# Optimization experiments

Hardware: AMD Instinct MI355X
Metric: run time of the kernel (lower is better)

## Reference

```python
import jax, jax.numpy as jnp
import numpy as np

T_STEP, NUM_PATCHES = 16, 49
DIM, MLP_DIM, HEADS, DEPTH = 512, 2048, 8, 4
PATCH_DIM = 432
N_BATCH = 32
NEG = -1e9
EPS = 1e-5


def _ln(x, g, b):
    m = x.mean(-1, keepdims=True)
    v = ((x - m) ** 2).mean(-1, keepdims=True)
    return (x - m) / jnp.sqrt(v + EPS) * g + b


def setup_inputs() -> dict:
    key = jax.random.key(0)
    ks = jax.random.split(key, 16)
    L = T_STEP * NUM_PATCHES
    s = 0.02
    return {
        "patch": jax.random.normal(ks[0], (N_BATCH, L, PATCH_DIM), jnp.float32),
        "done": jax.random.randint(ks[1], (N_BATCH, T_STEP - 1), 0, 2).astype(jnp.int32),
        "W_embed": jax.random.normal(ks[2], (PATCH_DIM, DIM), jnp.float32) * s,
        "b_embed": jnp.zeros((DIM,), jnp.float32),
        "spatial_embed": jax.random.normal(ks[3], (1, NUM_PATCHES, DIM), jnp.float32),
        "temporal_embed": jax.random.normal(ks[4], (1, T_STEP, DIM), jnp.float32),
        "ln1_g": jnp.ones((DEPTH, DIM), jnp.float32),
        "ln1_b": jnp.zeros((DEPTH, DIM), jnp.float32),
        "Wqkv": jax.random.normal(ks[5], (DEPTH, DIM, 3 * DIM), jnp.float32) * s,
        "bqkv": jnp.zeros((DEPTH, 3 * DIM), jnp.float32),
        "Wo": jax.random.normal(ks[6], (DEPTH, DIM, DIM), jnp.float32) * s,
        "bo": jnp.zeros((DEPTH, DIM), jnp.float32),
        "ln2_g": jnp.ones((DEPTH, DIM), jnp.float32),
        "ln2_b": jnp.zeros((DEPTH, DIM), jnp.float32),
        "W1": jax.random.normal(ks[7], (DEPTH, DIM, MLP_DIM), jnp.float32) * s,
        "b1": jnp.zeros((DEPTH, MLP_DIM), jnp.float32),
        "W2": jax.random.normal(ks[8], (DEPTH, MLP_DIM, DIM), jnp.float32) * s,
        "b2": jnp.zeros((DEPTH, DIM), jnp.float32),
        "out_g": jnp.ones((DIM,), jnp.float32),
        "out_b": jnp.zeros((DIM,), jnp.float32),
    }


def reference(patch, done, W_embed, b_embed, spatial_embed, temporal_embed,
              ln1_g, ln1_b, Wqkv, bqkv, Wo, bo, ln2_g, ln2_b,
              W1, b1, W2, b2, out_g, out_b):
    N, L, _ = patch.shape
    # patch embed + factored pos embed
    x = patch @ W_embed + b_embed
    pos = jnp.tile(spatial_embed, (1, T_STEP, 1)) + jnp.repeat(temporal_embed, NUM_PATCHES, axis=1)
    x = x + pos
    # episodic attention mask: done_mask[n,t] = 1 iff any done[n, c]==1 for c >= t
    d = done.astype(jnp.float32)  # (N, T-1)
    dm = (jnp.flip(jnp.cumsum(jnp.flip(d, 1), 1), 1) > 0).astype(jnp.float32)
    dm = jnp.concatenate([dm, jnp.zeros((N, 1), jnp.float32)], axis=1)  # (N, T)
    pm = jnp.repeat(dm, NUM_PATCHES, axis=1)  # (N, L)
    keep = 1.0 - pm
    mask = 1.0 - keep[:, :, None] * keep[:, None, :]  # (N, L, L); 1 = blocked
    bias = jnp.where(mask > 0.5, NEG, 0.0)[:, None, :, :]  # (N, 1, L, L)
    dh = DIM // HEADS
    scale = dh ** -0.5
    for i in range(DEPTH):
        h = _ln(x, ln1_g[i], ln1_b[i])
        qkv = h @ Wqkv[i] + bqkv[i]
        q, k, v = jnp.split(qkv, 3, axis=-1)
        q = q.reshape(N, L, HEADS, dh).transpose(0, 2, 1, 3)
        k = k.reshape(N, L, HEADS, dh).transpose(0, 2, 1, 3)
        v = v.reshape(N, L, HEADS, dh).transpose(0, 2, 1, 3)
        scores = jnp.einsum('nhqd,nhkd->nhqk', q, k) * scale + bias
        attn = jax.nn.softmax(scores, axis=-1)
        o = jnp.einsum('nhqk,nhkd->nhqd', attn, v)
        o = o.transpose(0, 2, 1, 3).reshape(N, L, DIM)
        x = x + (o @ Wo[i] + bo[i])
        h = _ln(x, ln2_g[i], ln2_b[i])
        x = x + (jax.nn.gelu(h @ W1[i] + b1[i], approximate=False) @ W2[i] + b2[i])
    return _ln(x, out_g, out_b)
```

## Files before the change

### kernel.cpp

```cpp
#include <hip/hip_runtime.h>
#include <math.h>

#define NB 32
#define LQ 784
#define LQP 832
#define DIM 512
#define HEADS 8
#define MLP 2048
#define KPAD 448
#define MROWS 25088

typedef __attribute__((ext_vector_type(8))) short s8v;
typedef __attribute__((ext_vector_type(4))) short s4v;
typedef __attribute__((ext_vector_type(4))) float f4v;

__device__ __forceinline__ short f2b(float f){
  unsigned u = __builtin_bit_cast(unsigned, f);
  u = (u + 0x7fffu + ((u >> 16) & 1u)) >> 16;
  return (short)u;
}
__device__ __forceinline__ float b2f(short s){
  unsigned u = ((unsigned)(unsigned short)s) << 16;
  return __builtin_bit_cast(float, u);
}

__device__ __forceinline__ void gll16(const short* g, short* l){
  __builtin_amdgcn_global_load_lds(
      (const __attribute__((address_space(1))) void*)g,
      (__attribute__((address_space(3))) void*)l, 16, 0, 0);
}

__device__ __forceinline__ void xcd_remap(int &bm, int &bn, int gx, int gy){
  int nwg = gx * gy;
  int flat = bm * gx + bn;
  int xcd = flat & 7, idx = flat >> 3;
  int q = nwg >> 3, r = nwg & 7;
  int nf = (xcd < r ? xcd * (q + 1) : r * (q + 1) + (xcd - r) * q) + idx;
  bm = nf / gx;
  bn = nf - bm * gx;
}

__global__ __launch_bounds__(512) void mask_k(const int* __restrict__ done, float* __restrict__ keepL,
                                              int* __restrict__ kmask, int* __restrict__ liveg){
  __shared__ float keep[32][16];
  int tid = threadIdx.x;
  { int n = tid >> 4, t = tid & 15;
    int any = 0;
    for (int c = t; c < 15; ++c) any |= done[n*15 + c];
    keep[n][t] = any ? 0.f : 1.f; }
  __syncthreads();
  for (int i = tid; i < NB*LQP; i += 512){
    int n = i / LQP, l = i - n*LQP;
    keepL[i] = (l < LQ) ? keep[n][l/49] : 0.f;
  }
  if (tid < 32){
    int n = tid, m = 0;
    for (int kb = 0; kb < 13; ++kb){
      int t0 = (kb*64)/49, t1 = (kb*64 + 63)/49; if (t1 > 15) t1 = 15;
      float a = 0.f;
      for (int t = t0; t <= t1; ++t) a += keep[n][t];
      if (a > 0.5f) m |= 1 << kb;
    }
    kmask[n] = m;
  }
  for (int g = tid; g < 392; g += 512){
    float a = 0.f;
    for (int i2 = 0; i2 < 64; ++i2){
      int row = g*64 + i2;
      int n = row / 784, l = row - n*784;
      a += keep[n][l/49];
    }
    liveg[g] = a > 0.5f ? 1 : 0;
  }
}

__global__ __launch_bounds__(256) void zpad_k(short* __restrict__ Qb, short* __restrict__ Kb,
                                              short* __restrict__ Vtb){
  int idx = blockIdx.x*256 + threadIdx.x;
  s8v z;
  #pragma unroll
  for (int e=0;e<8;++e) z[e] = 0;
  if (idx < 98304){
    int nh = idx / 384, r = idx - nh*384;
    *(s8v*)(Qb + (long)nh*LQP*64 + 784*64 + r*8) = z;
  } else if (idx < 196608){
    int i2 = idx - 98304; int nh = i2 / 384, r = i2 - nh*384;
    *(s8v*)(Kb + (long)nh*LQP*64 + 784*64 + r*8) = z;
  } else {
    int i2 = idx - 196608; int nh = i2 / 384, rem = i2 - nh*384, d = rem/6, s = rem - d*6;
    *(s8v*)(Vtb + ((long)nh*64 + d)*LQP + 784 + s*8) = z;
  }
}

__global__ __launch_bounds__(256) void vmean_k(const short* __restrict__ Vtb, float* __restrict__ Vm){
  int nh = blockIdx.x;
  int tid = threadIdx.x;
  int d = tid >> 2, seg = tid & 3;
  const short* row = Vtb + ((long)nh*64 + d)*LQP;
  float s = 0.f;
  for (int c = seg; c < 98; c += 4){
    s8v v = *(const s8v*)(row + c*8);
    #pragma unroll
    for (int e=0;e<8;++e) s += b2f(v[e]);
  }
  s += __shfl_xor(s, 1, 64);
  s += __shfl_xor(s, 2, 64);
  if (seg == 0) Vm[nh*64 + d] = s * (1.0f/784.0f);
}

__device__ __forceinline__ void transp_body(long idx, const float* __restrict__ src,
                                            short* __restrict__ dst, int R, int C, int Rpad,
                                            long sStride, long dStride){
  long per = (long)C * Rpad;
  int z = (int)(idx / per);
  long rem = idx - (long)z * per;
  int cc = (int)(rem / Rpad);
  int r  = (int)(rem - (long)cc * Rpad);
  short v = 0;
  if (r < R) v = f2b(src[(long)z * sStride + (long)r * C + cc]);
  dst[(long)z * dStride + rem] = v;
}

#define PB0 43904
#define PB1 896
#define PB2 12288
#define PB3 4096
#define PB4 16384
#define PB5 16384

__global__ __launch_bounds__(256) void prep_k(
    const float* __restrict__ patch, short* __restrict__ patchb,
    const float* __restrict__ Wemb, short* __restrict__ Wembt,
    const float* __restrict__ Wqkv, short* __restrict__ Wqkvt,
    const float* __restrict__ Wo, short* __restrict__ Wot,
    const float* __restrict__ W1, short* __restrict__ W1t,
    const float* __restrict__ W2, short* __restrict__ W2t){
  int b = blockIdx.x;
  int tid = threadIdx.x;
  if (b < PB0){
    long idx = (long)b*256 + tid;
    if (idx >= (long)MROWS*KPAD) return;
    int r = (int)(idx / KPAD);
    int c = (int)(idx - (long)r*KPAD);
    patchb[idx] = (c < 432) ? f2b(patch[(long)r*432 + c]) : (short)0;
  } else if (b < PB0+PB1){
    long idx = (long)(b-PB0)*256 + tid;
    if (idx < 229376) transp_body(idx, Wemb, Wembt, 432, 512, 448, 0, 0);
  } else if (b < PB0+PB1+PB2){
    long idx = (long)(b-PB0-PB1)*256 + tid;
    if (idx < 3145728) transp_body(idx, Wqkv, Wqkvt, 512, 1536, 512, 512L*1536, 1536L*512);
  } else if (b < PB0+PB1+PB2+PB3){
    long idx = (long)(b-PB0-PB1-PB2)*256 + tid;
    if (idx < 1048576) transp_body(idx, Wo, Wot, 512, 512, 512, 512L*512, 512L*512);
  } else if (b < PB0+PB1+PB2+PB3+PB4){
    long idx = (long)(b-PB0-PB1-PB2-PB3)*256 + tid;
    if (idx < 4194304) transp_body(idx, W1, W1t, 512, 2048, 512, 512L*2048, 2048L*512);
  } else {
    long idx = (long)(b-PB0-PB1-PB2-PB3-PB4)*256 + tid;
    if (idx < 4194304) transp_body(idx, W2, W2t, 2048, 512, 2048, 2048L*512, 512L*2048);
  }
}

__global__ __launch_bounds__(256) void ln_k(const float* __restrict__ x, const float* __restrict__ g,
                                            const float* __restrict__ b, short* __restrict__ outb,
                                            float* __restrict__ outf){
  int lane = threadIdx.x & 63;
  long row = (long)blockIdx.x * 4 + (threadIdx.x >> 6);
  const float* xr = x + row * DIM + lane * 8;
  float va[8];
  { float4 t0 = *(const float4*)xr; float4 t1 = *(const float4*)(xr + 4);
    va[0]=t0.x; va[1]=t0.y; va[2]=t0.z; va[3]=t0.w;
    va[4]=t1.x; va[5]=t1.y; va[6]=t1.z; va[7]=t1.w; }
  float s = 0.f, q = 0.f;
  #pragma unroll
  for (int j=0;j<8;++j){ s += va[j]; q += va[j]*va[j]; }
  #pragma unroll
  for (int m=1;m<64;m<<=1){ s += __shfl_xor(s,m,64); q += __shfl_xor(q,m,64); }
  float mean = s * (1.0f/DIM);
  float var = q * (1.0f/DIM) - mean*mean;
  float inv = rsqrtf(var + 1e-5f);
  int cb = lane*8;
  if (outb){
    s8v o;
    #pragma unroll
    for (int j=0;j<8;++j) o[j] = f2b((va[j]-mean)*inv*g[cb+j] + b[cb+j]);
    *(s8v*)(outb + row*DIM + cb) = o;
  } else {
    float4 t0, t1;
    t0.x=(va[0]-mean)*inv*g[cb+0]+b[cb+0]; t0.y=(va[1]-mean)*inv*g[cb+1]+b[cb+1];
    t0.z=(va[2]-mean)*inv*g[cb+2]+b[cb+2]; t0.w=(va[3]-mean)*inv*g[cb+3]+b[cb+3];
    t1.x=(va[4]-mean)*inv*g[cb+4]+b[cb+4]; t1.y=(va[5]-mean)*inv*g[cb+5]+b[cb+5];
    t1.z=(va[6]-mean)*inv*g[cb+6]+b[cb+6]; t1.w=(va[7]-mean)*inv*g[cb+7]+b[cb+7];
    *(float4*)(outf + row*DIM + cb) = t0;
    *(float4*)(outf + row*DIM + cb + 4) = t1;
  }
}

template<int EPI>
__global__ __launch_bounds__(256) void gemm_k(
    const short* __restrict__ A, const short* __restrict__ Bt,
    const float* __restrict__ bias, int K, int N,
    float* __restrict__ xres, short* __restrict__ outb,
    const float* __restrict__ sp, const float* __restrict__ tp,
    short* __restrict__ Qb, short* __restrict__ Kb, short* __restrict__ Vtb,
    const int* __restrict__ liveg)
{
  __shared__ __align__(16) short lA[2][128*64];
  __shared__ __align__(16) short lB[2][128*64];
  int bm = blockIdx.y, bn = blockIdx.x;
  xcd_remap(bm, bn, gridDim.x, gridDim.y);
  if (EPI == 1){
    if (bn < 8 && liveg[2*bm] == 0 && liveg[2*bm+1] == 0) return;
  }
  int tid = threadIdx.x;
  int lane = tid & 63, wid = tid >> 6;
  int col = lane & 15, quad = lane >> 4;
  int wm = (wid >> 1) * 64, wn = (wid & 1) * 64;
  f4v acc[4][4];
  #pragma unroll
  for (int i=0;i<4;++i)
    #pragma unroll
    for (int j=0;j<4;++j)
      #pragma unroll
      for (int e=0;e<4;++e) acc[i][j][e] = 0.0f;
  const short* Abase = A + (long)bm*128*K;
  const short* Bbase = Bt + (long)bn*128*K;
  int nt = K >> 6;
  #pragma unroll
  for (int c = 0; c < 4; ++c){
    int v = c*256 + tid;
    int r = v >> 3, j = v & 7;
    int kc = (j ^ (r & 7)) * 8;
    gll16(Abase + (long)r*K + kc, lA[0] + v*8);
    gll16(Bbase + (long)r*K + kc, lB[0] + v*8);
  }
  for (int t = 0; t < nt; ++t){
    int cur = t & 1;
    __builtin_amdgcn_s_barrier();
    __builtin_amdgcn_sched_barrier(0);
    if (t + 1 < nt){
      int kt = (t + 1) << 6;
      #pragma unroll
      for (int c = 0; c < 4; ++c){
        int v = c*256 + tid;
        int r = v >> 3, j = v & 7;
        int kc = (j ^ (r & 7)) * 8;
        gll16(Abase + (long)r*K + kt + kc, lA[cur^1] + v*8);
        gll16(Bbase + (long)r*K + kt + kc, lB[cur^1] + v*8);
      }
      asm volatile("s_waitcnt vmcnt(8)" ::: "memory");
    } else {
      asm volatile("s_waitcnt vmcnt(0)" ::: "memory");
    }
    __builtin_amdgcn_s_barrier();
    __builtin_amdgcn_sched_barrier(0);
    __builtin_amdgcn_s_setprio(1);
    #pragma unroll
    for (int ks = 0; ks < 2; ++ks){
      s8v af[4], bf[4];
      #pragma unroll
      for (int j=0;j<4;++j)
        af[j] = *(const s8v*)&lA[cur][(wm + j*16 + col)*64 + (((ks*4+quad) ^ (col&7)))*8];
      #pragma unroll
      for (int i=0;i<4;++i)
        bf[i] = *(const s8v*)&lB[cur][(wn + i*16 + col)*64 + (((ks*4+quad) ^ (col&7)))*8];
      #pragma unroll
      for (int i=0;i<4;++i)
        #pragma unroll
        for (int j=0;j<4;++j)
          acc[i][j] = __builtin_amdgcn_mfma_f32_16x16x32_bf16(bf[i], af[j], acc[i][j], 0, 0, 0);
    }
    __builtin_amdgcn_s_setprio(0);
    __builtin_amdgcn_sched_barrier(0);
  }
  #pragma unroll
  for (int j=0;j<4;++j){
    int grow = (int)bm*128 + wm + j*16 + col;
    int l = 0, t = 0, p = 0, n = 0;
    if (EPI == 0){ l = grow % LQ; t = l / 49; p = l - t*49; }
    if (EPI == 1){ n = grow / LQ; l = grow - n*LQ; }
    #pragma unroll
    for (int i=0;i<4;++i){
      int gc0 = (int)bn*128 + wn + i*16 + quad*4;
      float4 b4 = *(const float4*)(bias + gc0);
      float v0 = acc[i][j][0] + b4.x;
      float v1 = acc[i][j][1] + b4.y;
      float v2 = acc[i][j][2] + b4.z;
      float v3 = acc[i][j][3] + b4.w;
      if (EPI == 0){
        float4 s4 = *(const float4*)(sp + p*DIM + gc0);
        float4 t4 = *(const float4*)(tp + t*DIM + gc0);
        float4 o; o.x = v0 + s4.x + t4.x; o.y = v1 + s4.y + t4.y;
        o.z = v2 + s4.z + t4.z; o.w = v3 + s4.w + t4.w;
        *(float4*)(xres + (long)grow*DIM + gc0) = o;
      } else if (EPI == 1){
        if (gc0 < 512){
          int hh = gc0 >> 6, d0 = gc0 & 63;
          s4v o; o[0]=f2b(v0); o[1]=f2b(v1); o[2]=f2b(v2); o[3]=f2b(v3);
          *(s4v*)(Qb + (((long)(n*HEADS + hh))*LQP + l)*64 + d0) = o;
        } else if (gc0 < 1024){
          int c2 = gc0 - 512; int hh = c2 >> 6, d0 = c2 & 63;
          s4v o; o[0]=f2b(v0); o[1]=f2b(v1); o[2]=f2b(v2); o[3]=f2b(v3);
          *(s4v*)(Kb + (((long)(n*HEADS + hh))*LQP + l)*64 + d0) = o;
        } else {
          int c2 = gc0 - 1024; int hh = c2 >> 6, d0 = c2 & 63;
          long base = ((long)(n*HEADS + hh))*64;
          Vtb[(base + d0+0)*LQP + l] = f2b(v0);
          Vtb[(base + d0+1)*LQP + l] = f2b(v1);
          Vtb[(base + d0+2)*LQP + l] = f2b(v2);
          Vtb[(base + d0+3)*LQP + l] = f2b(v3);
        }
      } else if (EPI == 2){
        float4 xo = *(const float4*)(xres + (long)grow*DIM + gc0);
        xo.x += v0; xo.y += v1; xo.z += v2; xo.w += v3;
        *(float4*)(xres + (long)grow*DIM + gc0) = xo;
      } else if (EPI == 3){
        float g0 = v0 / (1.0f + __expf(-1.595769122f * v0 * (1.0f + 0.044715f*v0*v0)));
        float g1 = v1 / (1.0f + __expf(-1.595769122f * v1 * (1.0f + 0.044715f*v1*v1)));
        float g2 = v2 / (1.0f + __expf(-1.595769122f * v2 * (1.0f + 0.044715f*v2*v2)));
        float g3 = v3 / (1.0f + __expf(-1.595769122f * v3 * (1.0f + 0.044715f*v3*v3)));
        s4v o; o[0]=f2b(g0); o[1]=f2b(g1); o[2]=f2b(g2); o[3]=f2b(g3);
        *(s4v*)(outb + (long)grow*MLP + gc0) = o;
      }
    }
  }
}

__global__ __launch_bounds__(256) void attn_k(
    const short* __restrict__ Qb, const short* __restrict__ Kb,
    const short* __restrict__ Vtb, const float* __restrict__ keepL,
    const int* __restrict__ kmask, const float* __restrict__ Vm,
    short* __restrict__ Ob)
{
  __shared__ __align__(16) short lK[64*64];
  __shared__ __align__(16) short lV[64*64];
  __shared__ __align__(16) short lP[4][16*72];
  int tid = threadIdx.x;
  int lane = tid & 63, wid = tid >> 6;
  int col = lane & 15, quad = lane >> 4;
  int qb = blockIdx.x, h = blockIdx.y, n = blockIdx.z;
  long nh = (long)n*HEADS + h;
  int smask = kmask[n];
  int qr0 = qb*64 + wid*16;
  float vmv[4];
  #pragma unroll
  for (int j=0;j<4;++j) vmv[j] = Vm[nh*64 + j*16 + col];

  if (!((smask >> qb) & 1)){
    #pragma unroll
    for (int j=0;j<4;++j){
      short ov = f2b(vmv[j]);
      #pragma unroll
      for (int r=0;r<4;++r){
        int l = qr0 + quad*4 + r;
        if (l < LQ) Ob[((long)n*LQ + l)*DIM + h*64 + j*16 + col] = ov;
      }
    }
    return;
  }

  const float* kl = keepL + n*LQP;
  const short* qp = Qb + (nh*LQP + qr0 + col)*64 + quad*8;
  s8v aq0 = *(const s8v*)qp;
  s8v aq1 = *(const s8v*)(qp + 32);
  float keepA = kl[qr0 + col];
  if (keepA < 0.5f){
    #pragma unroll
    for (int e=0;e<8;++e){ aq0[e] = 0; aq1[e] = 0; }
  }
  float keepQ[4];
  #pragma unroll
  for (int r=0;r<4;++r) keepQ[r] = kl[qr0 + quad*4 + r];
  float kqs = keepQ[0] + keepQ[1] + keepQ[2] + keepQ[3];
  bool wlive = __ballot(kqs > 0.5f) != 0ull;
  float lsum[4] = {0.f,0.f,0.f,0.f};
  f4v Oacc[4];
  #pragma unroll
  for (int j=0;j<4;++j)
    #pragma unroll
    for (int e=0;e<4;++e) Oacc[j][e] = 0.0f;

  for (int kb = 0; kb < 13; ++kb){
    if (!((smask >> kb) & 1)) continue;
    int kbase = kb*64;
    __syncthreads();
    #pragma unroll
    for (int c = 0; c < 2; ++c){
      int v = c*256 + tid;
      int r = v >> 3, j = v & 7;
      int kc = (j ^ (r & 7)) * 8;
      gll16(Kb + (nh*LQP + kbase + r)*64 + kc, lK + v*8);
    }
    #pragma unroll
    for (int c = 0; c < 2; ++c){
      int v = c*256 + tid;
      int d = v >> 3, j = v & 7;
      int c8 = (j ^ (d & 7)) * 8;
      gll16(Vtb + (nh*64 + d)*LQP + kbase + c8, lV + v*8);
    }
    __syncthreads();
    if (!wlive) continue;
    float pm[4][4];
    #pragma unroll
    for (int ct = 0; ct < 4; ++ct){
      float keepK = kl[kbase + ct*16 + col];
      f4v s;
      #pragma unroll
      for (int e=0;e<4;++e) s[e] = 0.0f;
      #pragma unroll
      for (int ks = 0; ks < 2; ++ks){
        s8v bk = *(const s8v*)&lK[(ct*16 + col)*64 + (((ks*4+quad) ^ (col&7)))*8];
        if (keepK < 0.5f){
          #pragma unroll
          for (int e=0;e<8;++e) bk[e] = 0;
        }
        s = __builtin_amdgcn_mfma_f32_16x16x32_bf16(ks ? aq1 : aq0, bk, s, 0, 0, 0);
      }
      #pragma unroll
      for (int r=0;r<4;++r){
        float a = keepQ[r] * keepK;
        float t = fmaf(s[r], 0.125f, 10000.0f);
        float p = __expf(fmaf(a, t, -10000.0f));
        pm[ct][r] = p;
        lsum[r] += p;
      }
    }
    #pragma unroll
    for (int ct=0; ct<4; ++ct)
      #pragma unroll
      for (int r=0;r<4;++r)
        lP[wid][(quad*4 + r)*72 + ct*16 + col] = f2b(pm[ct][r]);
    #pragma unroll
    for (int j=0;j<4;++j){
      #pragma unroll
      for (int ks=0; ks<2; ++ks){
        s8v ap = *(const s8v*)&lP[wid][col*72 + ks*32 + quad*8];
        s8v bv = *(const s8v*)&lV[(j*16 + col)*64 + (((ks*4+quad) ^ (col&7)))*8];
        Oacc[j] = __builtin_amdgcn_mfma_f32_16x16x32_bf16(ap, bv, Oacc[j], 0, 0, 0);
      }
    }
  }
  #pragma unroll
  for (int m=1; m<16; m<<=1){
    #pragma unroll
    for (int r=0;r<4;++r) lsum[r] += __shfl_xor(lsum[r], m, 64);
  }
  float invl[4];
  #pragma unroll
  for (int r=0;r<4;++r) invl[r] = 1.0f / lsum[r];
  #pragma unroll
  for (int j=0;j<4;++j)
    #pragma unroll
    for (int r=0;r<4;++r){
      int l = qr0 + quad*4 + r;
      if (l < LQ){
        float val = keepQ[r] > 0.5f ? Oacc[j][r] * invl[r] : vmv[j];
        Ob[((long)n*LQ + l)*DIM + h*64 + j*16 + col] = f2b(val);
      }
    }
}

extern "C" void kernel_launch(void* const* d_in, const int* in_sizes, int n_in,
                              void* d_out, int out_size, void* d_ws, size_t ws_size,
                              hipStream_t stream) {
  const float* patch    = (const float*)d_in[0];
  const int*   done     = (const int*)d_in[1];
  const float* W_embed  = (const float*)d_in[2];
  const float* b_embed  = (const float*)d_in[3];
  const float* spatial  = (const float*)d_in[4];
  const float* temporal = (const float*)d_in[5];
  const float* ln1_g    = (const float*)d_in[6];
  const float* ln1_b    = (const float*)d_in[7];
  const float* Wqkv     = (const float*)d_in[8];
  const float* bqkv     = (const float*)d_in[9];
  const float* Wo       = (const float*)d_in[10];
  const float* bo       = (const float*)d_in[11];
  const float* ln2_g    = (const float*)d_in[12];
  const float* ln2_b    = (const float*)d_in[13];
  const float* W1       = (const float*)d_in[14];
  const float* b1       = (const float*)d_in[15];
  const float* W2       = (const float*)d_in[16];
  const float* b2       = (const float*)d_in[17];
  const float* out_g    = (const float*)d_in[18];
  const float* out_b    = (const float*)d_in[19];
  float* out = (float*)d_out;

  char* ws = (char*)d_ws;
  size_t off = 0;
  auto alloc = [&](size_t bytes)->char*{ char* p = ws + off; off += (bytes + 255) & ~(size_t)255; return p; };
  const size_t QKV_B = (size_t)NB*HEADS*LQP*64*2;
  float* x    = (float*)alloc((size_t)MROWS*DIM*4);
  short* hbuf = (short*)alloc((size_t)MROWS*DIM*2);
  char*  U    = alloc((size_t)MROWS*MLP*2);
  short* patchb = (short*)U;
  short* Qb   = (short*)U;
  short* Kbf  = (short*)(U + QKV_B);
  short* Vtb  = (short*)(U + 2*QKV_B);
  short* obuf = hbuf;
  short* mid  = (short*)U;
  short* Wembt = (short*)alloc((size_t)512*448*2);
  short* Wqkvt = (short*)alloc((size_t)4*1536*512*2);
  short* Wot   = (short*)alloc((size_t)4*512*512*2);
  short* W1t   = (short*)alloc((size_t)4*2048*512*2);
  short* W2t   = (short*)alloc((size_t)4*512*2048*2);
  float* keepL = (float*)alloc((size_t)NB*LQP*4);
  int*   kmask = (int*)alloc(NB*4);
  int*   liveg = (int*)alloc(392*4);
  float* Vm    = (float*)alloc((size_t)NB*HEADS*64*4);

  mask_k<<<1, 512, 0, stream>>>(done, keepL, kmask, liveg);
  prep_k<<<PB0+PB1+PB2+PB3+PB4+PB5, 256, 0, stream>>>(
      patch, patchb, W_embed, Wembt, Wqkv, Wqkvt, Wo, Wot, W1, W1t, W2, W2t);

  gemm_k<0><<<dim3(DIM/128, MROWS/128), 256, 0, stream>>>(
      patchb, Wembt, b_embed, KPAD, DIM, x, nullptr, spatial, temporal,
      nullptr, nullptr, nullptr, nullptr);

  zpad_k<<<1152, 256, 0, stream>>>(Qb, Kbf, Vtb);

  for (int i = 0; i < 4; ++i){
    ln_k<<<MROWS/4, 256, 0, stream>>>(x, ln1_g + i*DIM, ln1_b + i*DIM, hbuf, nullptr);
    gemm_k<1><<<dim3(1536/128, MROWS/128), 256, 0, stream>>>(
        hbuf, Wqkvt + (size_t)i*1536*512, bqkv + (size_t)i*1536, DIM, 1536,
        nullptr, nullptr, nullptr, nullptr, Qb, Kbf, Vtb, liveg);
    vmean_k<<<NB*HEADS, 256, 0, stream>>>(Vtb, Vm);
    attn_k<<<dim3(13, HEADS, NB), 256, 0, stream>>>(Qb, Kbf, Vtb, keepL, kmask, Vm, obuf);
    gemm_k<2><<<dim3(DIM/128, MROWS/128), 256, 0, stream>>>(
        obuf, Wot + (size_t)i*512*512, bo + (size_t)i*DIM, DIM, DIM,
        x, nullptr, nullptr, nullptr, nullptr, nullptr, nullptr, nullptr);
    ln_k<<<MROWS/4, 256, 0, stream>>>(x, ln2_g + i*DIM, ln2_b + i*DIM, hbuf, nullptr);
    gemm_k<3><<<dim3(MLP/128, MROWS/128), 256, 0, stream>>>(
        hbuf, W1t + (size_t)i*2048*512, b1 + (size_t)i*MLP, DIM, MLP,
        nullptr, mid, nullptr, nullptr, nullptr, nullptr, nullptr, nullptr);
    gemm_k<2><<<dim3(DIM/128, MROWS/128), 256, 0, stream>>>(
        mid, W2t + (size_t)i*512*2048, b2 + (size_t)i*DIM, MLP, DIM,
        x, nullptr, nullptr, nullptr, nullptr, nullptr, nullptr, nullptr);
  }
  ln_k<<<MROWS/4, 256, 0, stream>>>(x, out_g, out_b, nullptr, out);
}
```

Measured before the change: 1.548 ms.

## Use LDS-tiled weight transposes and a direct-B-load GEMM for MLP up-projection

Splits the patch conversion and the weight transposes into separate kernels. The transposes now go through a 64x64 shared-memory tile, so global reads and writes are both coalesced instead of strided. Adds a GEMM variant for the W1 projection that stages only A in double-buffered LDS and loads B fragments straight from global memory into registers. This halves LDS footprint to allow three blocks per CU, but makes B reads go through cache without LDS reuse.

```diff
diff --git a/kernel.cpp b/kernel.cpp
--- a/kernel.cpp
+++ b/kernel.cpp
@@ -108,56 +108,61 @@
   if (seg == 0) Vm[nh*64 + d] = s * (1.0f/784.0f);
 }
 
-__device__ __forceinline__ void transp_body(long idx, const float* __restrict__ src,
-                                            short* __restrict__ dst, int R, int C, int Rpad,
-                                            long sStride, long dStride){
-  long per = (long)C * Rpad;
-  int z = (int)(idx / per);
-  long rem = idx - (long)z * per;
-  int cc = (int)(rem / Rpad);
-  int r  = (int)(rem - (long)cc * Rpad);
-  short v = 0;
-  if (r < R) v = f2b(src[(long)z * sStride + (long)r * C + cc]);
-  dst[(long)z * dStride + rem] = v;
-}
-
 #define PB0 43904
-#define PB1 896
-#define PB2 12288
-#define PB3 4096
-#define PB4 16384
-#define PB5 16384
-
 __global__ __launch_bounds__(256) void prep_k(
-    const float* __restrict__ patch, short* __restrict__ patchb,
+    const float* __restrict__ patch, short* __restrict__ patchb){
+  long idx = (long)blockIdx.x*256 + threadIdx.x;
+  if (idx >= (long)MROWS*KPAD) return;
+  int r = (int)(idx / KPAD);
+  int c = (int)(idx - (long)r*KPAD);
+  patchb[idx] = (c < 432) ? f2b(patch[(long)r*432 + c]) : (short)0;
+}
+
+__device__ __forceinline__ void tile_tr(const float* __restrict__ src, short* __restrict__ dst,
+                                        int R, int C, int Rpad, int tr, int tc, int tid,
+                                        float (*tile)[65]){
+  int r0 = tr*64, c0 = tc*64;
+  int w = tid >> 6, lane = tid & 63;
+  #pragma unroll
+  for (int p = 0; p < 16; ++p){
+    int r = r0 + p*4 + w;
+    tile[p*4 + w][lane] = (r < R) ? src[(long)r*C + c0 + lane] : 0.f;
+  }
+  __syncthreads();
+  #pragma unroll
+  for (int p = 0; p < 16; ++p){
+    int cc = p*4 + w;
+    dst[(long)(c0 + cc)*Rpad + r0 + lane] = f2b(tile[lane][cc]);
+  }
+}
+
+__global__ __launch_bounds__(256) void trans_k(
     const float* __restrict__ Wemb, short* __restrict__ Wembt,
     const float* __restrict__ Wqkv, short* __restrict__ Wqkvt,
-    const float* __restrict__ Wo, short* __restrict__ Wot,
-    const float* __restrict__ W1, short* __restrict__ W1t,
-    const float* __restrict__ W2, short* __restrict__ W2t){
-  int b = blockIdx.x;
-  int tid = threadIdx.x;
-  if (b < PB0){
-    long idx = (long)b*256 + tid;
-    if (idx >= (long)MROWS*KPAD) return;
-    int r = (int)(idx / KPAD);
-    int c = (int)(idx - (long)r*KPAD);
-    patchb[idx] = (c < 432) ? f2b(patch[(long)r*432 + c]) : (short)0;
-  } else if (b < PB0+PB1){
-    long idx = (long)(b-PB0)*256 + tid;
-    if (idx < 229376) transp_body(idx, Wemb, Wembt, 432, 512, 448, 0, 0);
-  } else if (b < PB0+PB1+PB2){
-    long idx = (long)(b-PB0-PB1)*256 + tid;
-    if (idx < 3145728) transp_body(idx, Wqkv, Wqkvt, 512, 1536, 512, 512L*1536, 1536L*512);
-  } else if (b < PB0+PB1+PB2+PB3){
-    long idx = (long)(b-PB0-PB1-PB2)*256 + tid;
-    if (idx < 1048576) transp_body(idx, Wo, Wot, 512, 512, 512, 512L*512, 512L*512);
-  } else if (b < PB0+PB1+PB2+PB3+PB4){
-    long idx = (long)(b-PB0-PB1-PB2-PB3)*256 + tid;
-    if (idx < 4194304) transp_body(idx, W1, W1t, 512, 2048, 512, 512L*2048, 2048L*512);
+    const float* __restrict__ Wo,  short* __restrict__ Wot,
+    const float* __restrict__ W1,  short* __restrict__ W1t,
+    const float* __restrict__ W2,  short* __restrict__ W2t){
+  __shared__ float tile[64][65];
+  int b = blockIdx.x, tid = threadIdx.x;
+  if (b < 56){
+    int tr = b >> 3, tc = b & 7;
+    tile_tr(Wemb, Wembt, 432, 512, 448, tr, tc, tid, tile);
+  } else if (b < 56 + 768){
+    int i = b - 56; int z = i / 192, rem = i - z*192;
+    int tr = rem / 24, tc = rem - tr*24;
+    tile_tr(Wqkv + (long)z*512*1536, Wqkvt + (long)z*1536*512, 512, 1536, 512, tr, tc, tid, tile);
+  } else if (b < 56 + 768 + 256){
+    int i = b - 824; int z = i >> 6, rem = i & 63;
+    int tr = rem >> 3, tc = rem & 7;
+    tile_tr(Wo + (long)z*512*512, Wot + (long)z*512*512, 512, 512, 512, tr, tc, tid, tile);
+  } else if (b < 56 + 768 + 256 + 1024){
+    int i = b - 1080; int z = i >> 8, rem = i & 255;
+    int tr = rem >> 5, tc = rem & 31;
+    tile_tr(W1 + (long)z*512*2048, W1t + (long)z*2048*512, 512, 2048, 512, tr, tc, tid, tile);
   } else {
-    long idx = (long)(b-PB0-PB1-PB2-PB3-PB4)*256 + tid;
-    if (idx < 4194304) transp_body(idx, W2, W2t, 2048, 512, 2048, 2048L*512, 512L*2048);
+    int i = b - 2104; int z = i >> 8, rem = i & 255;
+    int tr = rem >> 3, tc = rem & 7;
+    tile_tr(W2 + (long)z*2048*512, W2t + (long)z*512*2048, 2048, 512, 2048, tr, tc, tid, tile);
   }
 }
 
@@ -326,6 +331,106 @@
   }
 }
 
+template<int EPI>
+__global__ __launch_bounds__(256, 3) void gemm_bd_k(
+    const short* __restrict__ A, const short* __restrict__ Bt,
+    const float* __restrict__ bias, int K, int N,
+    float* __restrict__ xres, short* __restrict__ outb)
+{
+  __shared__ __align__(16) short lA[2][128*64];
+  int bm = blockIdx.y, bn = blockIdx.x;
+  xcd_remap(bm, bn, gridDim.x, gridDim.y);
+  int tid = threadIdx.x;
+  int lane = tid & 63, wid = tid >> 6;
+  int col = lane & 15, quad = lane >> 4;
+  int wm = (wid >> 1) * 64, wn = (wid & 1) * 64;
+  f4v acc[4][4];
+  #pragma unroll
+  for (int i=0;i<4;++i)
+    #pragma unroll
+    for (int j=0;j<4;++j)
+      #pragma unroll
+      for (int e=0;e<4;++e) acc[i][j][e] = 0.0f;
+  const short* Abase = A + (long)bm*128*K;
+  int nt = K >> 6;
+  #pragma unroll
+  for (int c = 0; c < 4; ++c){
+    int v = c*256 + tid;
+    int r = v >> 3, j = v & 7;
+    int kc = (j ^ (r & 7)) * 8;
+    gll16(Abase + (long)r*K + kc, lA[0] + v*8);
+  }
+  for (int t = 0; t < nt; ++t){
+    int cur = t & 1;
+    __builtin_amdgcn_s_barrier();
+    __builtin_amdgcn_sched_barrier(0);
+    s8v bf[4][2];
+    {
+      int kt0 = t << 6;
+      #pragma unroll
+      for (int i=0;i<4;++i)
+        #pragma unroll
+        for (int ks=0;ks<2;++ks)
+          bf[i][ks] = *(const s8v*)(Bt + (long)(bn*128 + wn + i*16 + col)*K + kt0 + (ks*4+quad)*8);
+    }
+    if (t + 1 < nt){
+      int kt = (t + 1) << 6;
+      #pragma unroll
+      for (int c = 0; c < 4; ++c){
+        int v = c*256 + tid;
+        int r = v >> 3, j = v & 7;
+        int kc = (j ^ (r & 7)) * 8;
+        gll16(Abase + (long)r*K + kt + kc, lA[cur^1] + v*8);
+      }
+      asm volatile("s_waitcnt vmcnt(4)" ::: "memory");
+    } else {
+      asm volatile("s_waitcnt vmcnt(0)" ::: "memory");
+    }
+    __builtin_amdgcn_s_barrier();
+    __builtin_amdgcn_sched_barrier(0);
+    __builtin_amdgcn_s_setprio(1);
+    #pragma unroll
+    for (int ks = 0; ks < 2; ++ks){
+      s8v af[4];
+      #pragma unroll
+      for (int j=0;j<4;++j)
+        af[j] = *(const s8v*)&lA[cur][(wm + j*16 + col)*64 + (((ks*4+quad) ^ (col&7)))*8];
+      #pragma unroll
+      for (int i=0;i<4;++i)
+        #pragma unroll
+        for (int j=0;j<4;++j)
+          acc[i][j] = __builtin_amdgcn_mfma_f32_16x16x32_bf16(bf[i][ks], af[j], acc[i][j], 0, 0, 0);
+    }
+    __builtin_amdgcn_s_setprio(0);
+    __builtin_amdgcn_sched_barrier(0);
+  }
+  #pragma unroll
+  for (int j=0;j<4;++j){
+    int grow = (int)bm*128 + wm + j*16 + col;
+    #pragma unroll
+    for (int i=0;i<4;++i){
+      int gc0 = (int)bn*128 + wn + i*16 + quad*4;
+      float4 b4 = *(const float4*)(bias + gc0);
+      float v0 = acc[i][j][0] + b4.x;
+      float v1 = acc[i][j][1] + b4.y;
+      float v2 = acc[i][j][2] + b4.z;
+      float v3 = acc[i][j][3] + b4.w;
+      if (EPI == 2){
+        float4 xo = *(const float4*)(xres + (long)grow*DIM + gc0);
+        xo.x += v0; xo.y += v1; xo.z += v2; xo.w += v3;
+        *(float4*)(xres + (long)grow*DIM + gc0) = xo;
+      } else {
+        float g0 = v0 / (1.0f + __expf(-1.595769122f * v0 * (1.0f + 0.044715f*v0*v0)));
+        float g1 = v1 / (1.0f + __expf(-1.595769122f * v1 * (1.0f + 0.044715f*v1*v1)));
+        float g2 = v2 / (1.0f + __expf(-1.595769122f * v2 * (1.0f + 0.044715f*v2*v2)));
+        float g3 = v3 / (1.0f + __expf(-1.595769122f * v3 * (1.0f + 0.044715f*v3*v3)));
+        s4v o; o[0]=f2b(g0); o[1]=f2b(g1); o[2]=f2b(g2); o[3]=f2b(g3);
+        *(s4v*)(outb + (long)grow*MLP + gc0) = o;
+      }
+    }
+  }
+}
+
 __global__ __launch_bounds__(256) void attn_k(
     const short* __restrict__ Qb, const short* __restrict__ Kb,
     const short* __restrict__ Vtb, const float* __restrict__ keepL,
@@ -509,8 +614,8 @@
   float* Vm    = (float*)alloc((size_t)NB*HEADS*64*4);
 
   mask_k<<<1, 512, 0, stream>>>(done, keepL, kmask, liveg);
-  prep_k<<<PB0+PB1+PB2+PB3+PB4+PB5, 256, 0, stream>>>(
-      patch, patchb, W_embed, Wembt, Wqkv, Wqkvt, Wo, Wot, W1, W1t, W2, W2t);
+  prep_k<<<PB0, 256, 0, stream>>>(patch, patchb);
+  trans_k<<<3128, 256, 0, stream>>>(W_embed, Wembt, Wqkv, Wqkvt, Wo, Wot, W1, W1t, W2, W2t);
 
   gemm_k<0><<<dim3(DIM/128, MROWS/128), 256, 0, stream>>>(
       patchb, Wembt, b_embed, KPAD, DIM, x, nullptr, spatial, temporal,
@@ -529,9 +634,9 @@
         obuf, Wot + (size_t)i*512*512, bo + (size_t)i*DIM, DIM, DIM,
         x, nullptr, nullptr, nullptr, nullptr, nullptr, nullptr, nullptr);
     ln_k<<<MROWS/4, 256, 0, stream>>>(x, ln2_g + i*DIM, ln2_b + i*DIM, hbuf, nullptr);
-    gemm_k<3><<<dim3(MLP/128, MROWS/128), 256, 0, stream>>>(
+    gemm_bd_k<3><<<dim3(MLP/128, MROWS/128), 256, 0, stream>>>(
         hbuf, W1t + (size_t)i*2048*512, b1 + (size_t)i*MLP, DIM, MLP,
-        nullptr, mid, nullptr, nullptr, nullptr, nullptr, nullptr, nullptr);
+        nullptr, mid);
     gemm_k<2><<<dim3(DIM/128, MROWS/128), 256, 0, stream>>>(
         mid, W2t + (size_t)i*512*2048, b2 + (size_t)i*DIM, MLP, DIM,
         x, nullptr, nullptr, nullptr, nullptr, nullptr, nullptr, nullptr);
```

Result: slower. 1.644 ms (+6.2%).
